# Performance work log

Hardware: AMD Instinct MI355X
Metric: run time of the kernel (lower is better)

## Reference

```python
import jax, jax.numpy as jnp
from jax import lax
import numpy as np

DN = ('NCHW', 'OIHW', 'NCHW')
PAD = [(1, 1), (1, 1)]  # padding=1 each side
STRIDE = (1, 1)


def setup_inputs() -> dict:
    key = jax.random.key(0)
    k0, k1, k2, k3, k4, k5 = jax.random.split(key, 6)
    B, Cin, Cout, H, W, K, FES = 32, 96, 144, 56, 56, 3, 3
    fan_main = Cin * K * K
    fan_extra = FES * K * K
    x = jax.random.normal(k0, (B, Cin, H, W), dtype=jnp.float32)
    extra_inputs = jax.random.normal(k1, (B, Cout * FES), dtype=jnp.float32)
    Wm = jax.random.normal(k2, (Cout, Cin, K, K), dtype=jnp.float32) / np.sqrt(fan_main)
    bm = jax.random.normal(k3, (Cout,), dtype=jnp.float32) * 0.01
    Wx = jax.random.normal(k4, (Cout, FES, K, K), dtype=jnp.float32) / np.sqrt(fan_extra)
    bx = jax.random.normal(k5, (Cout,), dtype=jnp.float32) * 0.01
    return {"x": x, "extra_inputs": extra_inputs, "Wm": Wm, "bm": bm, "Wx": Wx, "bx": bx}


def reference(x, extra_inputs, Wm, bm, Wx, bx):
    # main path: standard conv + bias
    main = lax.conv_general_dilated(x, Wm, STRIDE, PAD, dimension_numbers=DN)
    main = main + bm[None, :, None, None]

    B = x.shape[0]
    Cout, FES, kh, kw = Wx.shape
    H2, W2 = main.shape[2], main.shape[3]

    # Extra path: each extra conv operates on a spatially-constant map, so
    # conv(const_c) = const_c * conv(ones). Compute per-(out,fes)-kernel response
    # to a ones map once (captures zero-padding boundary effects exactly),
    # then combine via a batched einsum — collapsing the per-channel loop.
    ones = jnp.ones((1, 1, x.shape[2], x.shape[3]), dtype=x.dtype)
    M = lax.conv_general_dilated(
        ones, Wx.reshape(Cout * FES, 1, kh, kw), STRIDE, PAD, dimension_numbers=DN
    )  # [1, Cout*FES, H2, W2]
    M = M.reshape(Cout, FES, H2, W2)

    extra = extra_inputs.reshape(B, Cout, FES)
    extra_out = jnp.einsum('bif,ifhw->bihw', extra, M) + bx[None, :, None, None]

    return main + extra_out
```

## Files before the change

kernel.cpp:

```cpp
#include <hip/hip_runtime.h>
#include <hip/hip_bf16.h>

#define B_    32
#define CIN   96
#define COUT  144
#define H_    56
#define W_    56
#define HW    3136
#define NPIX  100352
#define KTOT  864
#define MT    128
#define TAPSZ (COUT*CIN)

typedef short  short8  __attribute__((ext_vector_type(8)));
typedef float  floatx4 __attribute__((ext_vector_type(4)));

__device__ __attribute__((aligned(64))) float g_zero[16];

__device__ __forceinline__ unsigned short f2bf(float f) {
    union { float f; unsigned int u; } v; v.f = f;
    unsigned int u = v.u;
    return (unsigned short)((u + 0x7FFFu + ((u >> 16) & 1u)) >> 16);
}

__device__ __forceinline__ void glds16(const void* g, void* l) {
    __builtin_amdgcn_global_load_lds(
        (const __attribute__((address_space(1))) unsigned int*)g,
        (__attribute__((address_space(3))) unsigned int*)l, 16, 0, 0);
}

#define TB 1568
#define WB 486
__global__ __launch_bounds__(256) void prep_all(const float* __restrict__ x,
                                                unsigned short* __restrict__ xT,
                                                const float* __restrict__ Wm,
                                                unsigned short* __restrict__ Wt,
                                                const float* __restrict__ extra,
                                                const float* __restrict__ Wx,
                                                const float* __restrict__ bm,
                                                const float* __restrict__ bx,
                                                float* __restrict__ E) {
    __shared__ __align__(16) unsigned short tile[64][CIN + 8];
    int blk = blockIdx.x;
    int t = threadIdx.x;
    if (blk < TB) {
        int b   = blk / 49;
        int hw0 = (blk % 49) * 64;
        const float* xb = x + (size_t)b * CIN * HW;
        for (int i = t; i < CIN * 16; i += 256) {
            int ci = i >> 4, seg = i & 15;
            float4 v = *(const float4*)(xb + (size_t)ci * HW + hw0 + seg * 4);
            int hwl = seg * 4;
            tile[hwl + 0][ci] = f2bf(v.x);
            tile[hwl + 1][ci] = f2bf(v.y);
            tile[hwl + 2][ci] = f2bf(v.z);
            tile[hwl + 3][ci] = f2bf(v.w);
        }
        __syncthreads();
        int row = t >> 2, part = t & 3;
        const uint4* s = (const uint4*)&tile[row][part * 24];
        uint4* d = (uint4*)(xT + ((size_t)b * HW + hw0 + row) * CIN + part * 24);
        d[0] = s[0]; d[1] = s[1]; d[2] = s[2];
    } else if (blk < TB + WB) {
        int i = (blk - TB) * 256 + t;
        int tap = i / TAPSZ;
        int rem = i - tap * TAPSZ;
        int co  = rem / CIN, ci = rem - co * CIN;
        Wt[i] = f2bf(Wm[((size_t)co * CIN + ci) * 9 + tap]);
    } else {
        int i = (blk - TB - WB) * 256 + t;
        int b = i / COUT, co = i - b * COUT;
        float base = bm[co] + bx[co];
        float m[3][3] = {{0,0,0},{0,0,0},{0,0,0}};
        for (int f = 0; f < 3; ++f) {
            float e = extra[(size_t)b * (COUT * 3) + co * 3 + f];
            const float* w = Wx + ((size_t)co * 3 + f) * 9;
            for (int rc = 0; rc < 3; ++rc) {
                int kh0 = (rc == 0) ? 1 : 0;
                int kh1 = (rc == 2) ? 1 : 2;
                for (int cc = 0; cc < 3; ++cc) {
                    int kw0 = (cc == 0) ? 1 : 0;
                    int kw1 = (cc == 2) ? 1 : 2;
                    float s = 0.f;
                    for (int kh = kh0; kh <= kh1; ++kh)
                        for (int kw = kw0; kw <= kw1; ++kw)
                            s += w[kh * 3 + kw];
                    m[rc][cc] += e * s;
                }
            }
        }
        float* dst = E + (size_t)i * 9;
        for (int rc = 0; rc < 3; ++rc)
            for (int cc = 0; cc < 3; ++cc)
                dst[rc * 3 + cc] = base + m[rc][cc];
    }
}

__global__ __launch_bounds__(256, 3) void conv_gemm(const unsigned short* __restrict__ xT,
                                                    const unsigned short* __restrict__ Wt,
                                                    const float* __restrict__ E,
                                                    float* __restrict__ out) {
    __shared__ __align__(16) unsigned char smem[52224];
    unsigned short* As = (unsigned short*)smem;
    unsigned short* Bs = (unsigned short*)(smem + 24576);

    int tid = threadIdx.x;
    int wv = tid >> 6, lane = tid & 63;
    int pixBase = blockIdx.x * MT;
    int r16 = lane & 15, q = lane >> 4;

    floatx4 acc[2][9];
    #pragma unroll
    for (int m = 0; m < 2; ++m)
        #pragma unroll
        for (int n = 0; n < 9; ++n)
            acc[m][n] = (floatx4){0.f, 0.f, 0.f, 0.f};

    int aIdx[6], aH[6], aW[6];
    #pragma unroll
    for (int j = 0; j < 6; ++j) {
        int l = tid + j * 256;
        int r = l / 12, s = l - r * 12;
        int g = s - (r % 12); if (g < 0) g += 12;
        int p = pixBase + r;
        aIdx[j] = p * CIN + g * 8;
        int hw = p % HW;
        aH[j] = hw / W_;
        aW[j] = hw - aH[j] * W_;
    }
    int bIdx[7];
    #pragma unroll
    for (int j = 0; j < 7; ++j) {
        int l = tid + j * 256;
        int r = l / 12, s = l - r * 12;
        int g = s - (r % 12); if (g < 0) g += 12;
        bIdx[j] = r * CIN + g * 8;
    }
    const bool bTail = (tid < 192);

    int aBase[2], s0a[2];
    #pragma unroll
    for (int m = 0; m < 2; ++m) {
        int row = wv * 32 + m * 16 + r16;
        aBase[m] = row * CIN;
        s0a[m] = (row + q) % 12;
    }
    int bBase[9], s0b[9];
    #pragma unroll
    for (int n = 0; n < 9; ++n) {
        int row = n * 16 + r16;
        bBase[n] = row * CIN;
        s0b[n] = (row + q) % 12;
    }

    for (int tap = 0; tap < 9; ++tap) {
        int dh = tap / 3 - 1, dw = tap - (tap / 3) * 3 - 1;
        int off96 = (dh * W_ + dw) * CIN;
        if (tap) __syncthreads();

        #pragma unroll
        for (int j = 0; j < 6; ++j) {
            bool valid = ((unsigned)(aH[j] + dh) < H_) && ((unsigned)(aW[j] + dw) < W_);
            const unsigned short* src = valid ? (xT + aIdx[j] + off96)
                                              : (const unsigned short*)g_zero;
            glds16(src, As + tid * 8 + j * 2048);
        }
        const unsigned short* wsrc = Wt + tap * TAPSZ;
        #pragma unroll
        for (int j = 0; j < 6; ++j)
            glds16(wsrc + bIdx[j], Bs + tid * 8 + j * 2048);
        if (bTail)
            glds16(wsrc + bIdx[6], Bs + tid * 8 + 6 * 2048);

        __builtin_amdgcn_s_waitcnt(0x0F70);
        __syncthreads();

        #pragma unroll
        for (int ks = 0; ks < 3; ++ks) {
            short8 a[2], bf[9];
            #pragma unroll
            for (int m = 0; m < 2; ++m) {
                int slot = s0a[m] + 4 * ks; if (slot >= 12) slot -= 12;
                a[m] = *(const short8*)&As[aBase[m] + slot * 8];
            }
            #pragma unroll
            for (int n = 0; n < 9; ++n) {
                int slot = s0b[n] + 4 * ks; if (slot >= 12) slot -= 12;
                bf[n] = *(const short8*)&Bs[bBase[n] + slot * 8];
            }
            #pragma unroll
            for (int n = 0; n < 9; ++n) {
                acc[0][n] = __builtin_amdgcn_mfma_f32_16x16x32_bf16(a[0], bf[n], acc[0][n], 0, 0, 0);
                acc[1][n] = __builtin_amdgcn_mfma_f32_16x16x32_bf16(a[1], bf[n], acc[1][n], 0, 0, 0);
            }
        }
    }

    __syncthreads();
    float* Ct = (float*)smem;

    int pB[2], pHW[2], pRC[2], pCC[2][4];
    #pragma unroll
    for (int m = 0; m < 2; ++m) {
        int p0 = pixBase + wv * 32 + m * 16 + q * 4;
        int b  = p0 / HW;
        int hw0 = p0 - b * HW;
        int h = hw0 / W_;
        int w0 = hw0 - h * W_;
        pB[m] = b; pHW[m] = hw0;
        pRC[m] = (h == 0) ? 0 : ((h == H_ - 1) ? 2 : 1);
        pCC[m][0] = (w0 == 0) ? 0 : ((w0 == W_ - 1) ? 2 : 1);
        pCC[m][1] = (w0 + 1 == W_ - 1) ? 2 : 1;
        pCC[m][2] = (w0 + 2 == W_ - 1) ? 2 : 1;
        pCC[m][3] = (w0 + 3 == W_ - 1) ? 2 : 1;
    }
    int coT = tid >> 4, px8 = (tid & 15) * 8;
    int pS = pixBase + px8;
    int bS = pS / HW;
    int hwS = pS - bS * HW;

    #pragma unroll
    for (int n = 0; n < 9; ++n) {
        if (n) __syncthreads();
        #pragma unroll
        for (int m = 0; m < 2; ++m) {
            int co = n * 16 + r16;
            const float* Eb = E + ((size_t)pB[m] * COUT + co) * 9 + pRC[m] * 3;
            float4 v;
            v.x = acc[m][n][0] + Eb[pCC[m][0]];
            v.y = acc[m][n][1] + Eb[pCC[m][1]];
            v.z = acc[m][n][2] + Eb[pCC[m][2]];
            v.w = acc[m][n][3] + Eb[pCC[m][3]];
            *(float4*)&Ct[r16 * 132 + wv * 32 + m * 16 + q * 4] = v;
        }
        __syncthreads();
        float4 v0 = *(const float4*)&Ct[coT * 132 + px8];
        float4 v1 = *(const float4*)&Ct[coT * 132 + px8 + 4];
        float* dst = out + ((size_t)bS * COUT + n * 16 + coT) * HW + hwS;
        *(float4*)dst = v0;
        *(float4*)(dst + 4) = v1;
    }
}

extern "C" void kernel_launch(void* const* d_in, const int* in_sizes, int n_in,
                              void* d_out, int out_size, void* d_ws, size_t ws_size,
                              hipStream_t stream) {
    const float* x     = (const float*)d_in[0];
    const float* extra = (const float*)d_in[1];
    const float* Wm    = (const float*)d_in[2];
    const float* bm    = (const float*)d_in[3];
    const float* Wx    = (const float*)d_in[4];
    const float* bx    = (const float*)d_in[5];
    float* out = (float*)d_out;

    const size_t XT_BYTES = (size_t)NPIX * CIN * 2;
    const size_t WT_BYTES = (size_t)COUT * KTOT * 2;
    const size_t E_BYTES  = (size_t)B_ * COUT * 9 * 4;
    if (ws_size < XT_BYTES + WT_BYTES + E_BYTES) return;

    unsigned short* xT = (unsigned short*)d_ws;
    unsigned short* Wt = (unsigned short*)((char*)d_ws + XT_BYTES);
    float*          E  = (float*)((char*)d_ws + XT_BYTES + WT_BYTES);

    prep_all<<<TB + WB + 18, 256, 0, stream>>>(x, xT, Wm, Wt, extra, Wx, bm, bx, E);
    conv_gemm<<<NPIX / MT, 256, 0, stream>>>(xT, Wt, E, out);
}
```

Baseline: 169.9 us.

## Double-buffer weights in LDS, load activations to registers, widen pixel tile

Doubles the pixel tile per block to 256 and holds four 16-row M fragments per wave. Activation fragments now go straight from global memory into registers, and the next tap's loads are prefetched while the current tap's MFMAs run. Weights are double-buffered in LDS, using a channel-group-major layout that replaces the rotated-slot indexing. The epilogue drops the LDS transpose and writes float4 directly to output, which gives less coalesced stores. The much larger register footprint (launch bounds 1 block) cuts occupancy and halves the grid size.

```diff
diff --git a/kernel.cpp b/kernel.cpp
--- a/kernel.cpp
+++ b/kernel.cpp
@@ -9,13 +9,13 @@
 #define HW    3136
 #define NPIX  100352
 #define KTOT  864
-#define MT    128
+#define MT    256
 #define TAPSZ (COUT*CIN)
 
 typedef short  short8  __attribute__((ext_vector_type(8)));
 typedef float  floatx4 __attribute__((ext_vector_type(4)));
 
-__device__ __attribute__((aligned(64))) float g_zero[16];
+__device__ __attribute__((aligned(64))) float g_zero[64];
 
 __device__ __forceinline__ unsigned short f2bf(float f) {
     union { float f; unsigned int u; } v; v.f = f;
@@ -96,149 +96,135 @@
     }
 }
 
-__global__ __launch_bounds__(256, 3) void conv_gemm(const unsigned short* __restrict__ xT,
+__global__ __launch_bounds__(256, 1) void conv_gemm(const unsigned short* __restrict__ xT,
                                                     const unsigned short* __restrict__ Wt,
                                                     const float* __restrict__ E,
                                                     float* __restrict__ out) {
-    __shared__ __align__(16) unsigned char smem[52224];
-    unsigned short* As = (unsigned short*)smem;
-    unsigned short* Bs = (unsigned short*)(smem + 24576);
+    __shared__ __align__(16) unsigned short Bs[2 * TAPSZ];
 
     int tid = threadIdx.x;
     int wv = tid >> 6, lane = tid & 63;
+    int r16 = lane & 15, q = lane >> 4;
     int pixBase = blockIdx.x * MT;
-    int r16 = lane & 15, q = lane >> 4;
-
-    floatx4 acc[2][9];
-    #pragma unroll
-    for (int m = 0; m < 2; ++m)
+
+    floatx4 acc[4][9];
+    #pragma unroll
+    for (int m = 0; m < 4; ++m)
         #pragma unroll
         for (int n = 0; n < 9; ++n)
             acc[m][n] = (floatx4){0.f, 0.f, 0.f, 0.f};
 
-    int aIdx[6], aH[6], aW[6];
-    #pragma unroll
-    for (int j = 0; j < 6; ++j) {
-        int l = tid + j * 256;
-        int r = l / 12, s = l - r * 12;
-        int g = s - (r % 12); if (g < 0) g += 12;
-        int p = pixBase + r;
-        aIdx[j] = p * CIN + g * 8;
+    int aIdx[4], hA[4], wA[4];
+    #pragma unroll
+    for (int ms = 0; ms < 4; ++ms) {
+        int p = pixBase + wv * 64 + ms * 16 + r16;
+        aIdx[ms] = p * CIN;
         int hw = p % HW;
-        aH[j] = hw / W_;
-        aW[j] = hw - aH[j] * W_;
-    }
-    int bIdx[7];
+        hA[ms] = hw / W_;
+        wA[ms] = hw - hA[ms] * W_;
+    }
+    const unsigned short* gz = (const unsigned short*)g_zero;
+
+    int bSrc[7];
     #pragma unroll
     for (int j = 0; j < 7; ++j) {
-        int l = tid + j * 256;
-        int r = l / 12, s = l - r * 12;
-        int g = s - (r % 12); if (g < 0) g += 12;
-        bIdx[j] = r * CIN + g * 8;
+        int s = tid + j * 256;
+        int g = s / COUT, co = s - g * COUT;
+        bSrc[j] = co * CIN + g * 8;
     }
     const bool bTail = (tid < 192);
 
-    int aBase[2], s0a[2];
-    #pragma unroll
-    for (int m = 0; m < 2; ++m) {
-        int row = wv * 32 + m * 16 + r16;
-        aBase[m] = row * CIN;
-        s0a[m] = (row + q) % 12;
-    }
-    int bBase[9], s0b[9];
-    #pragma unroll
-    for (int n = 0; n < 9; ++n) {
-        int row = n * 16 + r16;
-        bBase[n] = row * CIN;
-        s0b[n] = (row + q) % 12;
-    }
-
+    const unsigned short* BpBase = Bs + (q * COUT + r16) * 8;
+
+    short8 a[2][4][3];
+
+    {
+        const unsigned short* wsrc = Wt;
+        #pragma unroll
+        for (int j = 0; j < 6; ++j)
+            glds16(wsrc + bSrc[j], (void*)(Bs + tid * 8 + j * 2048));
+        if (bTail)
+            glds16(wsrc + bSrc[6], (void*)(Bs + tid * 8 + 6 * 2048));
+        const int dh = -1, dw = -1, off = (dh * W_ + dw) * CIN;
+        #pragma unroll
+        for (int ms = 0; ms < 4; ++ms) {
+            bool valid = ((unsigned)(hA[ms] + dh) < H_) && ((unsigned)(wA[ms] + dw) < W_);
+            const unsigned short* base = valid ? (xT + aIdx[ms] + off) : gz;
+            #pragma unroll
+            for (int ks = 0; ks < 3; ++ks)
+                a[0][ms][ks] = *(const short8*)(base + ks * 32 + q * 8);
+        }
+    }
+    __syncthreads();
+
+    #pragma unroll
     for (int tap = 0; tap < 9; ++tap) {
-        int dh = tap / 3 - 1, dw = tap - (tap / 3) * 3 - 1;
-        int off96 = (dh * W_ + dw) * CIN;
-        if (tap) __syncthreads();
-
-        #pragma unroll
-        for (int j = 0; j < 6; ++j) {
-            bool valid = ((unsigned)(aH[j] + dh) < H_) && ((unsigned)(aW[j] + dw) < W_);
-            const unsigned short* src = valid ? (xT + aIdx[j] + off96)
-                                              : (const unsigned short*)g_zero;
-            glds16(src, As + tid * 8 + j * 2048);
-        }
-        const unsigned short* wsrc = Wt + tap * TAPSZ;
-        #pragma unroll
-        for (int j = 0; j < 6; ++j)
-            glds16(wsrc + bIdx[j], Bs + tid * 8 + j * 2048);
-        if (bTail)
-            glds16(wsrc + bIdx[6], Bs + tid * 8 + 6 * 2048);
-
-        __builtin_amdgcn_s_waitcnt(0x0F70);
+        const int cur = tap & 1, nxt = cur ^ 1;
+
+        if (tap < 8) {
+            const int tap2 = tap + 1;
+            const int dh2 = tap2 / 3 - 1, dw2 = tap2 - (tap2 / 3) * 3 - 1;
+            const unsigned short* wsrc = Wt + tap2 * TAPSZ;
+            unsigned short* bd = Bs + nxt * TAPSZ;
+            #pragma unroll
+            for (int j = 0; j < 6; ++j)
+                glds16(wsrc + bSrc[j], (void*)(bd + tid * 8 + j * 2048));
+            if (bTail)
+                glds16(wsrc + bSrc[6], (void*)(bd + tid * 8 + 6 * 2048));
+            const int off2 = (dh2 * W_ + dw2) * CIN;
+            #pragma unroll
+            for (int ms = 0; ms < 4; ++ms) {
+                bool valid = ((unsigned)(hA[ms] + dh2) < H_) && ((unsigned)(wA[ms] + dw2) < W_);
+                const unsigned short* base = valid ? (xT + aIdx[ms] + off2) : gz;
+                #pragma unroll
+                for (int ks = 0; ks < 3; ++ks)
+                    a[nxt][ms][ks] = *(const short8*)(base + ks * 32 + q * 8);
+            }
+        }
+
+        const unsigned short* Bp = BpBase + cur * TAPSZ;
+        #pragma unroll
+        for (int ks = 0; ks < 3; ++ks) {
+            short8 bf[9];
+            #pragma unroll
+            for (int n = 0; n < 9; ++n)
+                bf[n] = *(const short8*)(Bp + ks * 4608 + n * 128);
+            #pragma unroll
+            for (int n = 0; n < 9; ++n)
+                #pragma unroll
+                for (int ms = 0; ms < 4; ++ms)
+                    acc[ms][n] = __builtin_amdgcn_mfma_f32_16x16x32_bf16(
+                        a[cur][ms][ks], bf[n], acc[ms][n], 0, 0, 0);
+        }
+
         __syncthreads();
-
-        #pragma unroll
-        for (int ks = 0; ks < 3; ++ks) {
-            short8 a[2], bf[9];
-            #pragma unroll
-            for (int m = 0; m < 2; ++m) {
-                int slot = s0a[m] + 4 * ks; if (slot >= 12) slot -= 12;
-                a[m] = *(const short8*)&As[aBase[m] + slot * 8];
-            }
-            #pragma unroll
-            for (int n = 0; n < 9; ++n) {
-                int slot = s0b[n] + 4 * ks; if (slot >= 12) slot -= 12;
-                bf[n] = *(const short8*)&Bs[bBase[n] + slot * 8];
-            }
-            #pragma unroll
-            for (int n = 0; n < 9; ++n) {
-                acc[0][n] = __builtin_amdgcn_mfma_f32_16x16x32_bf16(a[0], bf[n], acc[0][n], 0, 0, 0);
-                acc[1][n] = __builtin_amdgcn_mfma_f32_16x16x32_bf16(a[1], bf[n], acc[1][n], 0, 0, 0);
-            }
-        }
-    }
-
-    __syncthreads();
-    float* Ct = (float*)smem;
-
-    int pB[2], pHW[2], pRC[2], pCC[2][4];
-    #pragma unroll
-    for (int m = 0; m < 2; ++m) {
-        int p0 = pixBase + wv * 32 + m * 16 + q * 4;
+    }
+
+    #pragma unroll
+    for (int ms = 0; ms < 4; ++ms) {
+        int p0 = pixBase + wv * 64 + ms * 16 + q * 4;
         int b  = p0 / HW;
         int hw0 = p0 - b * HW;
         int h = hw0 / W_;
         int w0 = hw0 - h * W_;
-        pB[m] = b; pHW[m] = hw0;
-        pRC[m] = (h == 0) ? 0 : ((h == H_ - 1) ? 2 : 1);
-        pCC[m][0] = (w0 == 0) ? 0 : ((w0 == W_ - 1) ? 2 : 1);
-        pCC[m][1] = (w0 + 1 == W_ - 1) ? 2 : 1;
-        pCC[m][2] = (w0 + 2 == W_ - 1) ? 2 : 1;
-        pCC[m][3] = (w0 + 3 == W_ - 1) ? 2 : 1;
-    }
-    int coT = tid >> 4, px8 = (tid & 15) * 8;
-    int pS = pixBase + px8;
-    int bS = pS / HW;
-    int hwS = pS - bS * HW;
-
-    #pragma unroll
-    for (int n = 0; n < 9; ++n) {
-        if (n) __syncthreads();
-        #pragma unroll
-        for (int m = 0; m < 2; ++m) {
+        int rc = (h == 0) ? 0 : ((h == H_ - 1) ? 2 : 1);
+        int cc0 = (w0 == 0) ? 0 : ((w0 == W_ - 1) ? 2 : 1);
+        int cc1 = (w0 + 1 == W_ - 1) ? 2 : 1;
+        int cc2 = (w0 + 2 == W_ - 1) ? 2 : 1;
+        int cc3 = (w0 + 3 == W_ - 1) ? 2 : 1;
+        const float* Ebase = E + (size_t)b * COUT * 9 + rc * 3;
+        float* outB = out + (size_t)b * COUT * HW + hw0;
+        #pragma unroll
+        for (int n = 0; n < 9; ++n) {
             int co = n * 16 + r16;
-            const float* Eb = E + ((size_t)pB[m] * COUT + co) * 9 + pRC[m] * 3;
+            const float* Eb = Ebase + co * 9;
             float4 v;
-            v.x = acc[m][n][0] + Eb[pCC[m][0]];
-            v.y = acc[m][n][1] + Eb[pCC[m][1]];
-            v.z = acc[m][n][2] + Eb[pCC[m][2]];
-            v.w = acc[m][n][3] + Eb[pCC[m][3]];
-            *(float4*)&Ct[r16 * 132 + wv * 32 + m * 16 + q * 4] = v;
-        }
-        __syncthreads();
-        float4 v0 = *(const float4*)&Ct[coT * 132 + px8];
-        float4 v1 = *(const float4*)&Ct[coT * 132 + px8 + 4];
-        float* dst = out + ((size_t)bS * COUT + n * 16 + coT) * HW + hwS;
-        *(float4*)dst = v0;
-        *(float4*)(dst + 4) = v1;
+            v.x = acc[ms][n][0] + Eb[cc0];
+            v.y = acc[ms][n][1] + Eb[cc1];
+            v.z = acc[ms][n][2] + Eb[cc2];
+            v.w = acc[ms][n][3] + Eb[cc3];
+            *(float4*)(outB + (size_t)co * HW) = v;
+        }
     }
 }
 
```

Measured after the change: 159.8 us. 1.06x faster.
